# Optimization experiments

Hardware: AMD Instinct MI355X
Metric: run time of the kernel (lower is better)

Reference implementation:

```python
import jax, jax.numpy as jnp
import numpy as np

N = 200000   # nodes
DEG = 32     # fixed padded degree
B = 16384    # batch of target nodes
D = 128      # feature dim (app/loc/time)
H = 128      # hidden dim
L = 5        # walk length (hard-coded in original forward)


def setup_inputs() -> dict:
    key = jax.random.key(0)
    ks = jax.random.split(key, 12)
    return {
        "x_app": jax.random.normal(ks[0], (N, D), jnp.float32),
        "x_loc": jax.random.normal(ks[1], (N, D), jnp.float32),
        "x_time": jax.random.normal(ks[2], (N, H), jnp.float32),
        "neighbors": jax.random.randint(ks[3], (N, DEG), 0, N, jnp.int32),
        "edge_weight": jax.random.uniform(ks[4], (N, DEG), jnp.float32, 1e-4, 1.0),
        "target_nodes": jax.random.randint(ks[5], (B,), 0, N, jnp.int32),
        "W_app": 0.05 * jax.random.normal(ks[6], (2 * D, H), jnp.float32),
        "b_app": jnp.zeros((H,), jnp.float32),
        "W_loc": 0.05 * jax.random.normal(ks[7], (2 * D, H), jnp.float32),
        "b_loc": jnp.zeros((H,), jnp.float32),
        "W_att": 0.05 * jax.random.normal(ks[8], (D + H, 1), jnp.float32),
        "b_att": jnp.zeros((1,), jnp.float32),
    }


def _walks(neighbors, edge_weight, start, key):
    """Batched weighted random walk. start: [B] -> walk node ids [B, L+1]."""
    def step(cur, k):
        nbrs = neighbors[cur]                 # [B, DEG] gather
        w = edge_weight[cur]                  # [B, DEG]
        # multinomial(prob,1) == categorical over log-weights
        c = jax.random.categorical(k, jnp.log(w), axis=-1)   # [B]
        nxt = jnp.take_along_axis(nbrs, c[:, None], axis=1)[:, 0]
        return nxt, nxt
    _, steps = jax.lax.scan(step, start, jax.random.split(key, L))  # steps: [L, B]
    return jnp.concatenate([start[None, :], steps], axis=0).T       # [B, L+1]


def reference(x_app, x_loc, x_time, neighbors, edge_weight, target_nodes,
              W_app, b_app, W_loc, b_loc, W_att, b_att):
    kw = jax.random.key(42)
    k1, k2 = jax.random.split(kw)
    app_walk = _walks(neighbors, edge_weight, target_nodes, k1)  # [B, L+1]
    loc_walk = _walks(neighbors, edge_weight, target_nodes, k2)  # [B, L+1]

    t_app = x_app[target_nodes]                                   # [B, D]
    t_loc = x_loc[target_nodes]                                   # [B, D]

    # SameTypeAggregator: sum neighbor feats, cat with target, Linear+ReLU
    f_app = jax.nn.relu(jnp.concatenate([t_app, x_app[app_walk].sum(axis=1)], axis=-1) @ W_app + b_app)
    f_loc = jax.nn.relu(jnp.concatenate([t_loc, x_loc[loc_walk].sum(axis=1)], axis=-1) @ W_loc + b_loc)

    # CrossTypeAttention over 3 feature types
    feats = jnp.stack([f_app, f_loc, x_time[target_nodes]], axis=0)      # [3, B, H]
    tgt = jnp.broadcast_to(t_app[None], (3,) + t_app.shape)              # [3, B, D]
    combined = jnp.concatenate([tgt, feats], axis=-1)                    # [3, B, D+H]
    scores = jax.nn.softmax(combined @ W_att + b_att, axis=0)            # [3, B, 1]
    return (scores * feats).sum(axis=0)                                  # [B, H]
```

## Files before the change

### kernel.cpp

```cpp
#include <hip/hip_runtime.h>
#include <stdint.h>

#define NN 200000
#define DEG 32
#define BB 16384
#define DD 128
#define HH 128
#define BM 64

typedef __attribute__((ext_vector_type(8))) short bf16x8;
typedef __attribute__((ext_vector_type(4))) float f32x4;

struct Keys { unsigned a[5][2]; unsigned l[5][2]; };

__host__ __device__ __forceinline__ unsigned rotl32(unsigned v, int r) {
  return (v << r) | (v >> (32 - r));
}

__host__ __device__ __forceinline__ void threefry2x32(
    unsigned k0, unsigned k1, unsigned x0, unsigned x1,
    unsigned* o0, unsigned* o1) {
  unsigned ks0 = k0, ks1 = k1, ks2 = k0 ^ k1 ^ 0x1BD11BDAu;
  x0 += ks0; x1 += ks1;
#define TF_RND(r) { x0 += x1; x1 = rotl32(x1, (r)); x1 ^= x0; }
  TF_RND(13) TF_RND(15) TF_RND(26) TF_RND(6)
  x0 += ks1; x1 += ks2 + 1u;
  TF_RND(17) TF_RND(29) TF_RND(16) TF_RND(24)
  x0 += ks2; x1 += ks0 + 2u;
  TF_RND(13) TF_RND(15) TF_RND(26) TF_RND(6)
  x0 += ks0; x1 += ks1 + 3u;
  TF_RND(17) TF_RND(29) TF_RND(16) TF_RND(24)
  x0 += ks1; x1 += ks2 + 4u;
  TF_RND(13) TF_RND(15) TF_RND(26) TF_RND(6)
  x0 += ks2; x1 += ks0 + 5u;
#undef TF_RND
  *o0 = x0; *o1 = x1;
}

__device__ __forceinline__ unsigned short f2bf(float x) {
  unsigned u = __float_as_uint(x);
  unsigned r = (u + 0x7fffu + ((u >> 16) & 1u)) >> 16;
  return (unsigned short)r;
}

__global__ __launch_bounds__(256) void walk_kernel(
    const int* __restrict__ neighbors, const float* __restrict__ ew,
    const int* __restrict__ target, int* __restrict__ walks, Keys keys) {
  int lane = threadIdx.x & 63;
  int sub = lane & 31;
  int grp = (int)((blockIdx.x * 256 + threadIdx.x) >> 5);
  int wk = grp >= BB ? 1 : 0;
  int b = grp - wk * BB;

  int cur = target[b];
  if (sub == 0) walks[(size_t)grp * 6] = cur;

  const float TINY = 1.17549435e-38f;

  for (int s = 0; s < 5; ++s) {
    int nb = neighbors[(size_t)cur * DEG + sub];
    float w = ew[(size_t)cur * DEG + sub];
    unsigned j = (unsigned)b * DEG + (unsigned)sub;
    unsigned k0 = wk ? keys.l[s][0] : keys.a[s][0];
    unsigned k1 = wk ? keys.l[s][1] : keys.a[s][1];
    unsigned y0, y1;
    threefry2x32(k0, k1, 0u, j, &y0, &y1);
    unsigned bits = y0 ^ y1;
    float f = __uint_as_float((bits >> 9) | 0x3f800000u) - 1.0f;
    float u = fmaxf(TINY, f + TINY);
    float g = -logf(-logf(u));
    float v = g + logf(w);
    int idx = sub;
    #pragma unroll
    for (int off = 16; off; off >>= 1) {
      float vo = __shfl_xor(v, off);
      int io = __shfl_xor(idx, off);
      if (vo > v || (vo == v && io < idx)) { v = vo; idx = io; }
    }
    cur = __shfl(nb, (lane & 32) + idx);
    if (sub == 0) walks[(size_t)grp * 6 + s + 1] = cur;
  }
}

__global__ __launch_bounds__(256) void prep_w(
    const float* __restrict__ Wapp, const float* __restrict__ Wloc,
    unsigned short* __restrict__ Wt) {
  int blk = blockIdx.x;
  int mat = blk >> 3;
  int k0 = (blk & 7) << 5;
  const float* W = mat ? Wloc : Wapp;
  __shared__ float tile[32][129];
  int t = threadIdx.x;
  #pragma unroll
  for (int i = 0; i < 16; ++i) {
    int idx = t + (i << 8);
    int kk = idx >> 7, n = idx & 127;
    tile[kk][n] = W[((size_t)(k0 + kk) << 7) + n];
  }
  __syncthreads();
  int n = t >> 1, h = (t & 1) << 4;
  unsigned pk[8];
  #pragma unroll
  for (int j = 0; j < 8; ++j) {
    float lo = tile[h + 2 * j][n];
    float hi = tile[h + 2 * j + 1][n];
    pk[j] = (unsigned)f2bf(lo) | ((unsigned)f2bf(hi) << 16);
  }
  unsigned short* dst = Wt + ((size_t)mat << 15) + ((size_t)n << 8) + k0 + h;
  uint4 lo4; lo4.x = pk[0]; lo4.y = pk[1]; lo4.z = pk[2]; lo4.w = pk[3];
  uint4 hi4; hi4.x = pk[4]; hi4.y = pk[5]; hi4.z = pk[6]; hi4.w = pk[7];
  reinterpret_cast<uint4*>(dst)[0] = lo4;
  reinterpret_cast<uint4*>(dst)[1] = hi4;
}

__global__ __launch_bounds__(256) void fuse2(
    const float* __restrict__ x_app, const float* __restrict__ x_loc,
    const float* __restrict__ x_time, const int* __restrict__ target,
    const int* __restrict__ walks, const unsigned short* __restrict__ Wt,
    const float* __restrict__ W_att, const float* __restrict__ b_att,
    const float* __restrict__ b_app, const float* __restrict__ b_loc,
    float* __restrict__ out) {
  __shared__ unsigned short sA[BM][264];
  __shared__ float attT[BM];

  int tid = threadIdx.x;
  int b0 = blockIdx.x * BM;
  int hw = tid >> 5;
  int c = tid & 31;

  #pragma unroll 2
  for (int it = 0; it < BM / 8; ++it) {
    int row = (it << 3) + hw;
    const int* wp = walks + (size_t)(b0 + row) * 6;
    int n0 = wp[0], n1 = wp[1], n2 = wp[2], n3 = wp[3], n4 = wp[4], n5 = wp[5];
    const float4 v0 = *(const float4*)&x_app[((size_t)n0 << 7) + 4 * c];
    const float4 v1 = *(const float4*)&x_app[((size_t)n1 << 7) + 4 * c];
    const float4 v2 = *(const float4*)&x_app[((size_t)n2 << 7) + 4 * c];
    const float4 v3 = *(const float4*)&x_app[((size_t)n3 << 7) + 4 * c];
    const float4 v4 = *(const float4*)&x_app[((size_t)n4 << 7) + 4 * c];
    const float4 v5 = *(const float4*)&x_app[((size_t)n5 << 7) + 4 * c];
    float sx = v0.x + v1.x + v2.x + v3.x + v4.x + v5.x;
    float sy = v0.y + v1.y + v2.y + v3.y + v4.y + v5.y;
    float sz = v0.z + v1.z + v2.z + v3.z + v4.z + v5.z;
    float sw = v0.w + v1.w + v2.w + v3.w + v4.w + v5.w;
    uint2 pt, ps;
    pt.x = (unsigned)f2bf(v0.x) | ((unsigned)f2bf(v0.y) << 16);
    pt.y = (unsigned)f2bf(v0.z) | ((unsigned)f2bf(v0.w) << 16);
    ps.x = (unsigned)f2bf(sx) | ((unsigned)f2bf(sy) << 16);
    ps.y = (unsigned)f2bf(sz) | ((unsigned)f2bf(sw) << 16);
    *(uint2*)&sA[row][4 * c] = pt;
    *(uint2*)&sA[row][128 + 4 * c] = ps;
    const float4 wa = *(const float4*)&W_att[4 * c];
    float p = v0.x * wa.x + v0.y * wa.y + v0.z * wa.z + v0.w * wa.w;
    #pragma unroll
    for (int off = 16; off; off >>= 1) p += __shfl_xor(p, off);
    if (c == 0) attT[row] = p;
  }
  __syncthreads();

  int w = tid >> 6;
  int l = tid & 63;
  int r15 = l & 15, g = l >> 4;
  int rowBase = w << 4;

  f32x4 accA[8];
  {
    bf16x8 aF[8];
    #pragma unroll
    for (int k = 0; k < 8; ++k)
      aF[k] = *(const bf16x8*)&sA[rowBase + r15][(k << 5) + (g << 3)];
    #pragma unroll
    for (int n = 0; n < 8; ++n) {
      f32x4 acc = {0.f, 0.f, 0.f, 0.f};
      #pragma unroll
      for (int k = 0; k < 8; ++k) {
        bf16x8 bF = *(const bf16x8*)&Wt[(((size_t)(n << 4) + r15) << 8) + (k << 5) + (g << 3)];
        acc = __builtin_amdgcn_mfma_f32_16x16x32_bf16(aF[k], bF, acc, 0, 0, 0);
      }
      accA[n] = acc;
    }
  }
  __syncthreads();

  #pragma unroll 2
  for (int it = 0; it < BM / 8; ++it) {
    int row = (it << 3) + hw;
    const int* wp = walks + (size_t)(BB + b0 + row) * 6;
    int n0 = wp[0], n1 = wp[1], n2 = wp[2], n3 = wp[3], n4 = wp[4], n5 = wp[5];
    const float4 v0 = *(const float4*)&x_loc[((size_t)n0 << 7) + 4 * c];
    const float4 v1 = *(const float4*)&x_loc[((size_t)n1 << 7) + 4 * c];
    const float4 v2 = *(const float4*)&x_loc[((size_t)n2 << 7) + 4 * c];
    const float4 v3 = *(const float4*)&x_loc[((size_t)n3 << 7) + 4 * c];
    const float4 v4 = *(const float4*)&x_loc[((size_t)n4 << 7) + 4 * c];
    const float4 v5 = *(const float4*)&x_loc[((size_t)n5 << 7) + 4 * c];
    float sx = v0.x + v1.x + v2.x + v3.x + v4.x + v5.x;
    float sy = v0.y + v1.y + v2.y + v3.y + v4.y + v5.y;
    float sz = v0.z + v1.z + v2.z + v3.z + v4.z + v5.z;
    float sw = v0.w + v1.w + v2.w + v3.w + v4.w + v5.w;
    uint2 pt, ps;
    pt.x = (unsigned)f2bf(v0.x) | ((unsigned)f2bf(v0.y) << 16);
    pt.y = (unsigned)f2bf(v0.z) | ((unsigned)f2bf(v0.w) << 16);
    ps.x = (unsigned)f2bf(sx) | ((unsigned)f2bf(sy) << 16);
    ps.y = (unsigned)f2bf(sz) | ((unsigned)f2bf(sw) << 16);
    *(uint2*)&sA[row][4 * c] = pt;
    *(uint2*)&sA[row][128 + 4 * c] = ps;
  }
  __syncthreads();

  f32x4 accL[8];
  {
    bf16x8 aF[8];
    #pragma unroll
    for (int k = 0; k < 8; ++k)
      aF[k] = *(const bf16x8*)&sA[rowBase + r15][(k << 5) + (g << 3)];
    const unsigned short* WtL = Wt + (1 << 15);
    #pragma unroll
    for (int n = 0; n < 8; ++n) {
      f32x4 acc = {0.f, 0.f, 0.f, 0.f};
      #pragma unroll
      for (int k = 0; k < 8; ++k) {
        bf16x8 bF = *(const bf16x8*)&WtL[(((size_t)(n << 4) + r15) << 8) + (k << 5) + (g << 3)];
        acc = __builtin_amdgcn_mfma_f32_16x16x32_bf16(aF[k], bF, acc, 0, 0, 0);
      }
      accL[n] = acc;
    }
  }

  float bA[8], bL[8], wv[8];
  #pragma unroll
  for (int n = 0; n < 8; ++n) {
    int col = (n << 4) + r15;
    bA[n] = b_app[col];
    bL[n] = b_loc[col];
    wv[n] = W_att[128 + col];
  }
  float batt = b_att[0];

  int trow[4];
  #pragma unroll
  for (int r = 0; r < 4; ++r) trow[r] = target[b0 + rowBase + (g << 2) + r];
  float tts[8][4];
  #pragma unroll
  for (int n = 0; n < 8; ++n)
    #pragma unroll
    for (int r = 0; r < 4; ++r)
      tts[n][r] = x_time[((size_t)trow[r] << 7) + (n << 4) + r15];

  #pragma unroll
  for (int r = 0; r < 4; ++r) {
    float fa[8], fl[8];
    float dA = 0.f, dL = 0.f, dT = 0.f;
    #pragma unroll
    for (int n = 0; n < 8; ++n) {
      fa[n] = fmaxf(accA[n][r] + bA[n], 0.f);
      fl[n] = fmaxf(accL[n][r] + bL[n], 0.f);
      dA += fa[n] * wv[n];
      dL += fl[n] * wv[n];
      dT += tts[n][r] * wv[n];
    }
    #pragma unroll
    for (int off = 1; off < 16; off <<= 1) {
      dA += __shfl_xor(dA, off);
      dL += __shfl_xor(dL, off);
      dT += __shfl_xor(dT, off);
    }
    float at = attT[rowBase + (g << 2) + r];
    float s0 = at + dA + batt;
    float s1 = at + dL + batt;
    float s2 = at + dT + batt;
    float m = fmaxf(s0, fmaxf(s1, s2));
    float e0 = expf(s0 - m), e1 = expf(s1 - m), e2 = expf(s2 - m);
    float inv = 1.f / (e0 + e1 + e2);
    size_t grow = (size_t)(b0 + rowBase + (g << 2) + r);
    #pragma unroll
    for (int n = 0; n < 8; ++n)
      out[(grow << 7) + (n << 4) + r15] = (e0 * fa[n] + e1 * fl[n] + e2 * tts[n][r]) * inv;
  }
}

extern "C" void kernel_launch(void* const* d_in, const int* in_sizes, int n_in,
                              void* d_out, int out_size, void* d_ws, size_t ws_size,
                              hipStream_t stream) {
  (void)in_sizes; (void)n_in; (void)out_size; (void)ws_size;
  const float* x_app   = (const float*)d_in[0];
  const float* x_loc   = (const float*)d_in[1];
  const float* x_time  = (const float*)d_in[2];
  const int*   neighbors = (const int*)d_in[3];
  const float* ew      = (const float*)d_in[4];
  const int*   target  = (const int*)d_in[5];
  const float* W_app   = (const float*)d_in[6];
  const float* b_app   = (const float*)d_in[7];
  const float* W_loc   = (const float*)d_in[8];
  const float* b_loc   = (const float*)d_in[9];
  const float* W_att   = (const float*)d_in[10];
  const float* b_att   = (const float*)d_in[11];
  float* out = (float*)d_out;
  int* walks = (int*)d_ws;
  unsigned short* Wt =
      (unsigned short*)((char*)d_ws + (size_t)2 * BB * 6 * sizeof(int));

  Keys keys;
  unsigned k1a, k1b, k2a, k2b;
  threefry2x32(0u, 42u, 0u, 0u, &k1a, &k1b);
  threefry2x32(0u, 42u, 0u, 1u, &k2a, &k2b);
  for (unsigned s = 0; s < 5; ++s) {
    threefry2x32(k1a, k1b, 0u, s, &keys.a[s][0], &keys.a[s][1]);
    threefry2x32(k2a, k2b, 0u, s, &keys.l[s][0], &keys.l[s][1]);
  }

  walk_kernel<<<(2 * BB * 32) / 256, 256, 0, stream>>>(neighbors, ew, target, walks, keys);
  prep_w<<<16, 256, 0, stream>>>(W_app, W_loc, Wt);
  fuse2<<<BB / BM, 256, 0, stream>>>(x_app, x_loc, x_time, target, walks, Wt,
                                     W_att, b_att, b_app, b_loc, out);
}
```

Before: 64.86 us.

## Shrink fused tile to 16 rows, split output columns across waves

The fused aggregation+attention kernel now handles 16 rows per block instead of 64, giving four times as many blocks. Each of the four waves computes a 32-column slice of both the app and loc GEMMs for the same 16 rows. The app and loc gathers are done together into separate shared buffers, which removes one of the two gather/GEMM phase barriers. Because the attention dot products are now split across waves, they are reduced through shared memory with an extra barrier, and every block reloads the full weight matrices. The intent is higher occupancy and more parallelism to hide gather latency, at the cost of more weight traffic per output row.

Measured after the change: 61.13 us. 1.06x faster.

```diff
diff --git a/kernel.cpp b/kernel.cpp
--- a/kernel.cpp
+++ b/kernel.cpp
@@ -6,7 +6,7 @@
 #define BB 16384
 #define DD 128
 #define HH 128
-#define BM 64
+#define BM 16
 
 typedef __attribute__((ext_vector_type(8))) short bf16x8;
 typedef __attribute__((ext_vector_type(4))) float f32x4;
@@ -113,7 +113,7 @@
   reinterpret_cast<uint4*>(dst)[1] = hi4;
 }
 
-__global__ __launch_bounds__(256) void fuse2(
+__global__ __launch_bounds__(256, 4) void fuse3(
     const float* __restrict__ x_app, const float* __restrict__ x_loc,
     const float* __restrict__ x_time, const int* __restrict__ target,
     const int* __restrict__ walks, const unsigned short* __restrict__ Wt,
@@ -121,115 +121,100 @@
     const float* __restrict__ b_app, const float* __restrict__ b_loc,
     float* __restrict__ out) {
   __shared__ unsigned short sA[BM][264];
+  __shared__ unsigned short sL[BM][264];
   __shared__ float attT[BM];
+  __shared__ float4 sRed[4][BM];
 
   int tid = threadIdx.x;
   int b0 = blockIdx.x * BM;
   int hw = tid >> 5;
   int c = tid & 31;
 
-  #pragma unroll 2
+  #pragma unroll
   for (int it = 0; it < BM / 8; ++it) {
     int row = (it << 3) + hw;
-    const int* wp = walks + (size_t)(b0 + row) * 6;
-    int n0 = wp[0], n1 = wp[1], n2 = wp[2], n3 = wp[3], n4 = wp[4], n5 = wp[5];
-    const float4 v0 = *(const float4*)&x_app[((size_t)n0 << 7) + 4 * c];
-    const float4 v1 = *(const float4*)&x_app[((size_t)n1 << 7) + 4 * c];
-    const float4 v2 = *(const float4*)&x_app[((size_t)n2 << 7) + 4 * c];
-    const float4 v3 = *(const float4*)&x_app[((size_t)n3 << 7) + 4 * c];
-    const float4 v4 = *(const float4*)&x_app[((size_t)n4 << 7) + 4 * c];
-    const float4 v5 = *(const float4*)&x_app[((size_t)n5 << 7) + 4 * c];
-    float sx = v0.x + v1.x + v2.x + v3.x + v4.x + v5.x;
-    float sy = v0.y + v1.y + v2.y + v3.y + v4.y + v5.y;
-    float sz = v0.z + v1.z + v2.z + v3.z + v4.z + v5.z;
-    float sw = v0.w + v1.w + v2.w + v3.w + v4.w + v5.w;
-    uint2 pt, ps;
-    pt.x = (unsigned)f2bf(v0.x) | ((unsigned)f2bf(v0.y) << 16);
-    pt.y = (unsigned)f2bf(v0.z) | ((unsigned)f2bf(v0.w) << 16);
-    ps.x = (unsigned)f2bf(sx) | ((unsigned)f2bf(sy) << 16);
-    ps.y = (unsigned)f2bf(sz) | ((unsigned)f2bf(sw) << 16);
-    *(uint2*)&sA[row][4 * c] = pt;
-    *(uint2*)&sA[row][128 + 4 * c] = ps;
-    const float4 wa = *(const float4*)&W_att[4 * c];
-    float p = v0.x * wa.x + v0.y * wa.y + v0.z * wa.z + v0.w * wa.w;
-    #pragma unroll
-    for (int off = 16; off; off >>= 1) p += __shfl_xor(p, off);
-    if (c == 0) attT[row] = p;
+    {
+      const int* wp = walks + (size_t)(b0 + row) * 6;
+      int n0 = wp[0], n1 = wp[1], n2 = wp[2], n3 = wp[3], n4 = wp[4], n5 = wp[5];
+      const float4 v0 = *(const float4*)&x_app[((size_t)n0 << 7) + 4 * c];
+      const float4 v1 = *(const float4*)&x_app[((size_t)n1 << 7) + 4 * c];
+      const float4 v2 = *(const float4*)&x_app[((size_t)n2 << 7) + 4 * c];
+      const float4 v3 = *(const float4*)&x_app[((size_t)n3 << 7) + 4 * c];
+      const float4 v4 = *(const float4*)&x_app[((size_t)n4 << 7) + 4 * c];
+      const float4 v5 = *(const float4*)&x_app[((size_t)n5 << 7) + 4 * c];
+      float sx = v0.x + v1.x + v2.x + v3.x + v4.x + v5.x;
+      float sy = v0.y + v1.y + v2.y + v3.y + v4.y + v5.y;
+      float sz = v0.z + v1.z + v2.z + v3.z + v4.z + v5.z;
+      float sw = v0.w + v1.w + v2.w + v3.w + v4.w + v5.w;
+      uint2 pt, ps;
+      pt.x = (unsigned)f2bf(v0.x) | ((unsigned)f2bf(v0.y) << 16);
+      pt.y = (unsigned)f2bf(v0.z) | ((unsigned)f2bf(v0.w) << 16);
+      ps.x = (unsigned)f2bf(sx) | ((unsigned)f2bf(sy) << 16);
+      ps.y = (unsigned)f2bf(sz) | ((unsigned)f2bf(sw) << 16);
+      *(uint2*)&sA[row][4 * c] = pt;
+      *(uint2*)&sA[row][128 + 4 * c] = ps;
+      const float4 wa = *(const float4*)&W_att[4 * c];
+      float p = v0.x * wa.x + v0.y * wa.y + v0.z * wa.z + v0.w * wa.w;
+      #pragma unroll
+      for (int off = 16; off; off >>= 1) p += __shfl_xor(p, off);
+      if (c == 0) attT[row] = p;
+    }
+    {
+      const int* wp = walks + (size_t)(BB + b0 + row) * 6;
+      int n0 = wp[0], n1 = wp[1], n2 = wp[2], n3 = wp[3], n4 = wp[4], n5 = wp[5];
+      const float4 v0 = *(const float4*)&x_loc[((size_t)n0 << 7) + 4 * c];
+      const float4 v1 = *(const float4*)&x_loc[((size_t)n1 << 7) + 4 * c];
+      const float4 v2 = *(const float4*)&x_loc[((size_t)n2 << 7) + 4 * c];
+      const float4 v3 = *(const float4*)&x_loc[((size_t)n3 << 7) + 4 * c];
+      const float4 v4 = *(const float4*)&x_loc[((size_t)n4 << 7) + 4 * c];
+      const float4 v5 = *(const float4*)&x_loc[((size_t)n5 << 7) + 4 * c];
+      float sx = v0.x + v1.x + v2.x + v3.x + v4.x + v5.x;
+      float sy = v0.y + v1.y + v2.y + v3.y + v4.y + v5.y;
+      float sz = v0.z + v1.z + v2.z + v3.z + v4.z + v5.z;
+      float sw = v0.w + v1.w + v2.w + v3.w + v4.w + v5.w;
+      uint2 pt, ps;
+      pt.x = (unsigned)f2bf(v0.x) | ((unsigned)f2bf(v0.y) << 16);
+      pt.y = (unsigned)f2bf(v0.z) | ((unsigned)f2bf(v0.w) << 16);
+      ps.x = (unsigned)f2bf(sx) | ((unsigned)f2bf(sy) << 16);
+      ps.y = (unsigned)f2bf(sz) | ((unsigned)f2bf(sw) << 16);
+      *(uint2*)&sL[row][4 * c] = pt;
+      *(uint2*)&sL[row][128 + 4 * c] = ps;
+    }
   }
   __syncthreads();
 
   int w = tid >> 6;
   int l = tid & 63;
   int r15 = l & 15, g = l >> 4;
-  int rowBase = w << 4;
-
-  f32x4 accA[8];
+
+  f32x4 accA[2], accL[2];
   {
-    bf16x8 aF[8];
-    #pragma unroll
-    for (int k = 0; k < 8; ++k)
-      aF[k] = *(const bf16x8*)&sA[rowBase + r15][(k << 5) + (g << 3)];
-    #pragma unroll
-    for (int n = 0; n < 8; ++n) {
-      f32x4 acc = {0.f, 0.f, 0.f, 0.f};
+    bf16x8 aF[8], lF[8];
+    #pragma unroll
+    for (int k = 0; k < 8; ++k) {
+      aF[k] = *(const bf16x8*)&sA[r15][(k << 5) + (g << 3)];
+      lF[k] = *(const bf16x8*)&sL[r15][(k << 5) + (g << 3)];
+    }
+    #pragma unroll
+    for (int n = 0; n < 2; ++n) {
+      int col = ((w << 1) + n) << 4;
+      f32x4 a1 = {0.f, 0.f, 0.f, 0.f}, a2 = {0.f, 0.f, 0.f, 0.f};
       #pragma unroll
       for (int k = 0; k < 8; ++k) {
-        bf16x8 bF = *(const bf16x8*)&Wt[(((size_t)(n << 4) + r15) << 8) + (k << 5) + (g << 3)];
-        acc = __builtin_amdgcn_mfma_f32_16x16x32_bf16(aF[k], bF, acc, 0, 0, 0);
+        bf16x8 bA = *(const bf16x8*)&Wt[(((size_t)col + r15) << 8) + (k << 5) + (g << 3)];
+        bf16x8 bL = *(const bf16x8*)&Wt[(1 << 15) + (((size_t)col + r15) << 8) + (k << 5) + (g << 3)];
+        a1 = __builtin_amdgcn_mfma_f32_16x16x32_bf16(aF[k], bA, a1, 0, 0, 0);
+        a2 = __builtin_amdgcn_mfma_f32_16x16x32_bf16(lF[k], bL, a2, 0, 0, 0);
       }
-      accA[n] = acc;
-    }
-  }
-  __syncthreads();
-
-  #pragma unroll 2
-  for (int it = 0; it < BM / 8; ++it) {
-    int row = (it << 3) + hw;
-    const int* wp = walks + (size_t)(BB + b0 + row) * 6;
-    int n0 = wp[0], n1 = wp[1], n2 = wp[2], n3 = wp[3], n4 = wp[4], n5 = wp[5];
-    const float4 v0 = *(const float4*)&x_loc[((size_t)n0 << 7) + 4 * c];
-    const float4 v1 = *(const float4*)&x_loc[((size_t)n1 << 7) + 4 * c];
-    const float4 v2 = *(const float4*)&x_loc[((size_t)n2 << 7) + 4 * c];
-    const float4 v3 = *(const float4*)&x_loc[((size_t)n3 << 7) + 4 * c];
-    const float4 v4 = *(const float4*)&x_loc[((size_t)n4 << 7) + 4 * c];
-    const float4 v5 = *(const float4*)&x_loc[((size_t)n5 << 7) + 4 * c];
-    float sx = v0.x + v1.x + v2.x + v3.x + v4.x + v5.x;
-    float sy = v0.y + v1.y + v2.y + v3.y + v4.y + v5.y;
-    float sz = v0.z + v1.z + v2.z + v3.z + v4.z + v5.z;
-    float sw = v0.w + v1.w + v2.w + v3.w + v4.w + v5.w;
-    uint2 pt, ps;
-    pt.x = (unsigned)f2bf(v0.x) | ((unsigned)f2bf(v0.y) << 16);
-    pt.y = (unsigned)f2bf(v0.z) | ((unsigned)f2bf(v0.w) << 16);
-    ps.x = (unsigned)f2bf(sx) | ((unsigned)f2bf(sy) << 16);
-    ps.y = (unsigned)f2bf(sz) | ((unsigned)f2bf(sw) << 16);
-    *(uint2*)&sA[row][4 * c] = pt;
-    *(uint2*)&sA[row][128 + 4 * c] = ps;
-  }
-  __syncthreads();
-
-  f32x4 accL[8];
-  {
-    bf16x8 aF[8];
-    #pragma unroll
-    for (int k = 0; k < 8; ++k)
-      aF[k] = *(const bf16x8*)&sA[rowBase + r15][(k << 5) + (g << 3)];
-    const unsigned short* WtL = Wt + (1 << 15);
-    #pragma unroll
-    for (int n = 0; n < 8; ++n) {
-      f32x4 acc = {0.f, 0.f, 0.f, 0.f};
-      #pragma unroll
-      for (int k = 0; k < 8; ++k) {
-        bf16x8 bF = *(const bf16x8*)&WtL[(((size_t)(n << 4) + r15) << 8) + (k << 5) + (g << 3)];
-        acc = __builtin_amdgcn_mfma_f32_16x16x32_bf16(aF[k], bF, acc, 0, 0, 0);
-      }
-      accL[n] = acc;
-    }
-  }
-
-  float bA[8], bL[8], wv[8];
-  #pragma unroll
-  for (int n = 0; n < 8; ++n) {
-    int col = (n << 4) + r15;
+      accA[n] = a1;
+      accL[n] = a2;
+    }
+  }
+
+  float bA[2], bL[2], wv[2];
+  #pragma unroll
+  for (int n = 0; n < 2; ++n) {
+    int col = (((w << 1) + n) << 4) + r15;
     bA[n] = b_app[col];
     bL[n] = b_loc[col];
     wv[n] = W_att[128 + col];
@@ -238,24 +223,24 @@
 
   int trow[4];
   #pragma unroll
-  for (int r = 0; r < 4; ++r) trow[r] = target[b0 + rowBase + (g << 2) + r];
-  float tts[8][4];
-  #pragma unroll
-  for (int n = 0; n < 8; ++n)
+  for (int r = 0; r < 4; ++r) trow[r] = target[b0 + (g << 2) + r];
+  float tts[2][4];
+  #pragma unroll
+  for (int n = 0; n < 2; ++n)
     #pragma unroll
     for (int r = 0; r < 4; ++r)
-      tts[n][r] = x_time[((size_t)trow[r] << 7) + (n << 4) + r15];
-
+      tts[n][r] = x_time[((size_t)trow[r] << 7) + (((w << 1) + n) << 4) + r15];
+
+  float fa[2][4], fl[2][4];
   #pragma unroll
   for (int r = 0; r < 4; ++r) {
-    float fa[8], fl[8];
     float dA = 0.f, dL = 0.f, dT = 0.f;
     #pragma unroll
-    for (int n = 0; n < 8; ++n) {
-      fa[n] = fmaxf(accA[n][r] + bA[n], 0.f);
-      fl[n] = fmaxf(accL[n][r] + bL[n], 0.f);
-      dA += fa[n] * wv[n];
-      dL += fl[n] * wv[n];
+    for (int n = 0; n < 2; ++n) {
+      fa[n][r] = fmaxf(accA[n][r] + bA[n], 0.f);
+      fl[n][r] = fmaxf(accL[n][r] + bL[n], 0.f);
+      dA += fa[n][r] * wv[n];
+      dL += fl[n][r] * wv[n];
       dT += tts[n][r] * wv[n];
     }
     #pragma unroll
@@ -264,17 +249,30 @@
       dL += __shfl_xor(dL, off);
       dT += __shfl_xor(dT, off);
     }
-    float at = attT[rowBase + (g << 2) + r];
-    float s0 = at + dA + batt;
-    float s1 = at + dL + batt;
-    float s2 = at + dT + batt;
+    if (r15 == 0) {
+      float4 q; q.x = dA; q.y = dL; q.z = dT; q.w = 0.f;
+      sRed[w][(g << 2) + r] = q;
+    }
+  }
+  __syncthreads();
+
+  #pragma unroll
+  for (int r = 0; r < 4; ++r) {
+    int row = (g << 2) + r;
+    float4 q0 = sRed[0][row], q1 = sRed[1][row], q2 = sRed[2][row], q3 = sRed[3][row];
+    float at = attT[row] + batt;
+    float s0 = at + q0.x + q1.x + q2.x + q3.x;
+    float s1 = at + q0.y + q1.y + q2.y + q3.y;
+    float s2 = at + q0.z + q1.z + q2.z + q3.z;
     float m = fmaxf(s0, fmaxf(s1, s2));
     float e0 = expf(s0 - m), e1 = expf(s1 - m), e2 = expf(s2 - m);
     float inv = 1.f / (e0 + e1 + e2);
-    size_t grow = (size_t)(b0 + rowBase + (g << 2) + r);
-    #pragma unroll
-    for (int n = 0; n < 8; ++n)
-      out[(grow << 7) + (n << 4) + r15] = (e0 * fa[n] + e1 * fl[n] + e2 * tts[n][r]) * inv;
+    size_t grow = (size_t)(b0 + row);
+    #pragma unroll
+    for (int n = 0; n < 2; ++n) {
+      int col = (((w << 1) + n) << 4) + r15;
+      out[(grow << 7) + col] = (e0 * fa[n][r] + e1 * fl[n][r] + e2 * tts[n][r]) * inv;
+    }
   }
 }
 
@@ -310,6 +308,6 @@
 
   walk_kernel<<<(2 * BB * 32) / 256, 256, 0, stream>>>(neighbors, ew, target, walks, keys);
   prep_w<<<16, 256, 0, stream>>>(W_app, W_loc, Wt);
-  fuse2<<<BB / BM, 256, 0, stream>>>(x_app, x_loc, x_time, target, walks, Wt,
+  fuse3<<<BB / BM, 256, 0, stream>>>(x_app, x_loc, x_time, target, walks, Wt,
                                      W_att, b_att, b_app, b_loc, out);
 }
```
